# Performance work log

Hardware: AMD Instinct MI355X
Metric: run time of the kernel (lower is better)

The kernel has to match this reference:

```python
import jax, jax.numpy as jnp
import numpy as np

N = 100000
E = 1000000
F_NODE = 64
F_EDGE = 32
H = 128
C_NODE = 12
C_EDGE = 4


def _glorot(key, shape):
    fan_in, fan_out = shape[0], shape[1]
    s = (6.0 / (fan_in + fan_out)) ** 0.5
    return jax.random.uniform(key, shape, jnp.float32, -s, s)


def setup_inputs() -> dict:
    key = jax.random.key(0)
    ks = jax.random.split(key, 16)
    x = jax.random.normal(ks[0], (N, F_NODE), jnp.float32)
    edge_index = jax.random.randint(ks[1], (2, E), 0, N, jnp.int32)
    edge_attr = jax.random.normal(ks[2], (E, F_EDGE), jnp.float32)
    return {
        "x": x,
        "edge_index": edge_index,
        "edge_attr": edge_attr,
        "We": _glorot(ks[3], (F_NODE, H)), "be": jnp.zeros((H,), jnp.float32),
        "Wc1": _glorot(ks[4], (H, H)), "bc1": jnp.zeros((H,), jnp.float32),
        "Wc2": _glorot(ks[5], (H, H)), "bc2": jnp.zeros((H,), jnp.float32),
        "Wn1": _glorot(ks[6], (H, H // 2)), "bn1": jnp.zeros((H // 2,), jnp.float32),
        "Wn2": _glorot(ks[7], (H // 2, C_NODE)), "bn2": jnp.zeros((C_NODE,), jnp.float32),
        "Wedge1": _glorot(ks[8], (2 * H + F_EDGE, H)), "bedge1": jnp.zeros((H,), jnp.float32),
        "Wedge2": _glorot(ks[9], (H, C_EDGE)), "bedge2": jnp.zeros((C_EDGE,), jnp.float32),
    }


def _gcn_conv(x, W, b, src, tgt, n):
    # PyG GCNConv: add self-loops, symmetric deg normalization, scatter-add.
    xw = x @ W  # [N, H]
    loop = jnp.arange(n, dtype=src.dtype)
    s = jnp.concatenate([src, loop])
    t = jnp.concatenate([tgt, loop])
    deg = jax.ops.segment_sum(jnp.ones_like(t, jnp.float32), t, num_segments=n)
    dinv = jnp.where(deg > 0, jax.lax.rsqrt(jnp.maximum(deg, 1.0)), 0.0)
    norm = dinv[s] * dinv[t]  # [E+N]
    msg = xw[s] * norm[:, None]
    return jax.ops.segment_sum(msg, t, num_segments=n) + b


def reference(x, edge_index, edge_attr, We, be, Wc1, bc1, Wc2, bc2,
              Wn1, bn1, Wn2, bn2, Wedge1, bedge1, Wedge2, bedge2):
    n = x.shape[0]
    row, col = edge_index[0], edge_index[1]
    h = jax.nn.relu(x @ We + be)          # node_embed Linear+ReLU
    h = jax.nn.relu(h)                     # extra F.relu in forward
    h = jax.nn.relu(_gcn_conv(h, Wc1, bc1, row, col, n))
    h = jax.nn.relu(_gcn_conv(h, Wc2, bc2, row, col, n))
    node_logits = jax.nn.relu(h @ Wn1 + bn1) @ Wn2 + bn2
    e = jnp.concatenate([h[row], h[col], edge_attr], axis=-1)  # [E, 2H+Fe]
    edge_logits = jax.nn.relu(e @ Wedge1 + bedge1) @ Wedge2 + bedge2
    return (node_logits, edge_logits)
```

## Files before the change

kernel.cpp:

```cpp
#include <hip/hip_runtime.h>

#define N_NODES 100000
#define N_EDGES 1000000
#define NB_SCAN 391
#define EDGE_OUT_BASE 1200000

typedef __attribute__((ext_vector_type(8))) short short8;
typedef __attribute__((ext_vector_type(4))) unsigned short us4;
typedef __attribute__((ext_vector_type(4))) float f32x4;

__device__ __forceinline__ float bf2f(unsigned short u) {
    unsigned int x = ((unsigned int)u) << 16;
    return __builtin_bit_cast(float, x);
}
__device__ __forceinline__ float lo_bf(unsigned int u) {
    return __builtin_bit_cast(float, u << 16);
}
__device__ __forceinline__ float hi_bf(unsigned int u) {
    return __builtin_bit_cast(float, u & 0xffff0000u);
}
__device__ __forceinline__ unsigned short f2bf(float f) {
    unsigned int x = __builtin_bit_cast(unsigned int, f);
    return (unsigned short)((x + 0x7fffu + ((x >> 16) & 1u)) >> 16);
}

__global__ __launch_bounds__(256) void k_detect(const unsigned short* __restrict__ xr,
                                                int* __restrict__ flag) {
    __shared__ int s[256];
    int t = threadIdx.x;
    int cnt = 0;
    for (int i = t; i < 8192; i += 256) {
        int e = (xr[i] >> 7) & 0xFF;
        if (e >= 148) cnt++;
    }
    s[t] = cnt;
    __syncthreads();
    for (int off = 128; off > 0; off >>= 1) {
        if (t < off) s[t] += s[t + off];
        __syncthreads();
    }
    if (t == 0) *flag = (s[0] > 100) ? 1 : 0;
}

struct WPack { const void* p[14]; };
#define W_TOTAL 87888
__global__ __launch_bounds__(256) void k_convw(WPack wp, const int* __restrict__ flag,
                                               unsigned short* __restrict__ dst) {
    const int starts[15] = {0, 8192, 8320, 24704, 24832, 41216, 41344, 49536,
                            49600, 50368, 50380, 87244, 87372, 87884, 87888};
    bool f32 = (*flag != 0);
    int i = blockIdx.x * 256 + threadIdx.x;
    if (i >= W_TOTAL) return;
    int s = 0;
#pragma unroll
    for (int k = 1; k < 14; k++) s += (i >= starts[k]) ? 1 : 0;
    int j = i - starts[s];
    dst[i] = f32 ? f2bf(((const float*)wp.p[s])[j]) : ((const unsigned short*)wp.p[s])[j];
}
#define OW_We 0
#define OW_be 8192
#define OW_Wc1 8320
#define OW_bc1 24704
#define OW_Wc2 24832
#define OW_bc2 41216
#define OW_Wn1 41344
#define OW_bn1 49536
#define OW_Wn2 49600
#define OW_bn2 50368
#define OW_We1 50380
#define OW_be1 87244
#define OW_We2 87372
#define OW_be2 87884

__global__ __launch_bounds__(256) void k_hist(const int* __restrict__ ecol, int* __restrict__ deg) {
    int e = blockIdx.x * 256 + threadIdx.x;
    if (e < N_EDGES) atomicAdd(&deg[ecol[e]], 1);
}

__global__ __launch_bounds__(256) void k_scanA(const int* __restrict__ deg, int* __restrict__ bsum) {
    __shared__ int s[256];
    int i = blockIdx.x * 256 + threadIdx.x;
    s[threadIdx.x] = (i < N_NODES) ? deg[i] : 0;
    __syncthreads();
    for (int off = 128; off > 0; off >>= 1) {
        if (threadIdx.x < off) s[threadIdx.x] += s[threadIdx.x + off];
        __syncthreads();
    }
    if (threadIdx.x == 0) bsum[blockIdx.x] = s[0];
}

__global__ __launch_bounds__(512) void k_scanB(int* __restrict__ bsum) {
    __shared__ int s[512];
    int t = threadIdx.x;
    int v = (t < NB_SCAN) ? bsum[t] : 0;
    s[t] = v;
    __syncthreads();
    for (int off = 1; off < 512; off <<= 1) {
        int x = (t >= off) ? s[t - off] : 0;
        __syncthreads();
        s[t] += x;
        __syncthreads();
    }
    if (t < NB_SCAN) bsum[t] = s[t] - v;
}

__global__ __launch_bounds__(256) void k_scanC(const int* __restrict__ deg, const int* __restrict__ bsum,
                                               int* __restrict__ row_off, int* __restrict__ cursor,
                                               float* __restrict__ dinv) {
    __shared__ int s[256];
    int i = blockIdx.x * 256 + threadIdx.x;
    int t = threadIdx.x;
    int v = (i < N_NODES) ? deg[i] : 0;
    s[t] = v;
    __syncthreads();
    for (int off = 1; off < 256; off <<= 1) {
        int x = (t >= off) ? s[t - off] : 0;
        __syncthreads();
        s[t] += x;
        __syncthreads();
    }
    int excl = s[t] - v + bsum[blockIdx.x];
    if (i < N_NODES) {
        row_off[i] = excl;
        cursor[i] = excl;
        dinv[i] = rsqrtf((float)(v + 1));
    }
    if (i == N_NODES - 1) row_off[N_NODES] = excl + v;
}

__global__ __launch_bounds__(256) void k_fill(const int* __restrict__ erow, const int* __restrict__ ecol,
                                              int* __restrict__ cursor, int* __restrict__ csr,
                                              int2* __restrict__ aux) {
    int e = blockIdx.x * 256 + threadIdx.x;
    if (e < N_EDGES) {
        int c = ecol[e];
        int pos = atomicAdd(&cursor[c], 1);
        csr[pos] = erow[e];
        aux[pos] = make_int2(e, c);
    }
}

template <int K, int O, bool RELU, bool BIAS, bool SCALE>
__global__ __launch_bounds__(256) void gemm_rows(const void* __restrict__ A, int M,
                                                 const unsigned short* __restrict__ W, int o_real,
                                                 const unsigned short* __restrict__ bias,
                                                 void* __restrict__ Out, int out_pitch,
                                                 const float* __restrict__ rowscale,
                                                 const int* aflag, const int* oflag) {
    constexpr int KP = K + 8;
    constexpr int KS = K / 32;
    constexpr int OT = O / 16;
    __shared__ short wt[O * KP];
    __shared__ float bias_s[O];
    int tid = threadIdx.x;
    for (int idx = tid; idx < K * O; idx += 256) {
        int k = idx / O, o = idx % O;
        short w = 0;
        if (o < o_real) w = (short)W[(size_t)k * o_real + o];
        wt[o * KP + k] = w;
    }
    if (BIAS) {
        for (int o = tid; o < O; o += 256) bias_s[o] = (o < o_real) ? bf2f(bias[o]) : 0.f;
    }
    __syncthreads();

    bool af32 = aflag && (*aflag != 0);
    bool of32 = oflag && (*oflag != 0);

    int wid = tid >> 6, lane = tid & 63;
    int rbase = (blockIdx.x * 4 + wid) * 32;
    if (rbase >= M) return;
    int lq = lane >> 4, lr = lane & 15;

    short8 a[2][KS];
#pragma unroll
    for (int rg = 0; rg < 2; rg++) {
        int row = rbase + rg * 16 + lr;
        if (row >= M) row = M - 1;
        if (af32) {
            const float* ap = (const float*)A + (size_t)row * K + lq * 8;
#pragma unroll
            for (int ks = 0; ks < KS; ks++) {
                f32x4 u0 = *(const f32x4*)(ap + ks * 32);
                f32x4 u1 = *(const f32x4*)(ap + ks * 32 + 4);
                short8 v;
                v[0] = (short)f2bf(u0[0]); v[1] = (short)f2bf(u0[1]);
                v[2] = (short)f2bf(u0[2]); v[3] = (short)f2bf(u0[3]);
                v[4] = (short)f2bf(u1[0]); v[5] = (short)f2bf(u1[1]);
                v[6] = (short)f2bf(u1[2]); v[7] = (short)f2bf(u1[3]);
                a[rg][ks] = v;
            }
        } else {
            const unsigned short* ap = (const unsigned short*)A + (size_t)row * K + lq * 8;
#pragma unroll
            for (int ks = 0; ks < KS; ks++) a[rg][ks] = *(const short8*)(ap + ks * 32);
        }
    }

    f32x4 acc[2][OT];
#pragma unroll
    for (int rg = 0; rg < 2; rg++)
#pragma unroll
        for (int j = 0; j < OT; j++) {
            acc[rg][j][0] = 0.f; acc[rg][j][1] = 0.f; acc[rg][j][2] = 0.f; acc[rg][j][3] = 0.f;
        }

#pragma unroll
    for (int j = 0; j < OT; j++) {
        short8 b[KS];
#pragma unroll
        for (int ks = 0; ks < KS; ks++)
            b[ks] = *(const short8*)(&wt[(lr + 16 * j) * KP + ks * 32 + lq * 8]);
#pragma unroll
        for (int rg = 0; rg < 2; rg++)
#pragma unroll
            for (int ks = 0; ks < KS; ks++)
                acc[rg][j] = __builtin_amdgcn_mfma_f32_16x16x32_bf16(a[rg][ks], b[ks], acc[rg][j], 0, 0, 0);
    }

#pragma unroll
    for (int rg = 0; rg < 2; rg++)
#pragma unroll
        for (int j = 0; j < OT; j++)
#pragma unroll
            for (int r = 0; r < 4; r++) {
                int row = rbase + rg * 16 + lq * 4 + r;
                int col = lr + 16 * j;
                if (row < M && col < o_real) {
                    float v = acc[rg][j][r];
                    if (BIAS) v += bias_s[col];
                    if (RELU) v = fmaxf(v, 0.f);
                    if (SCALE) v *= rowscale[row];
                    size_t oi = (size_t)row * out_pitch + col;
                    if (of32) ((float*)Out)[oi] = v;
                    else ((unsigned short*)Out)[oi] = f2bf(v);
                }
            }
}

__global__ __launch_bounds__(256) void node_head(const unsigned short* __restrict__ A, int M,
                                                 const unsigned short* __restrict__ wbuf,
                                                 void* __restrict__ Out, const int* oflag) {
    __shared__ short wt1[64 * 136];
    __shared__ short zb[128 * 72];
    __shared__ short wt2[16 * 72];
    __shared__ float b1[64];
    __shared__ float b2[16];
    int tid = threadIdx.x;
    const unsigned short* Wn1 = wbuf + OW_Wn1;
    const unsigned short* Wn2 = wbuf + OW_Wn2;
    for (int idx = tid; idx < 64 * 128; idx += 256) {
        int k = idx >> 6, o = idx & 63;
        wt1[o * 136 + k] = (short)Wn1[idx];
    }
    for (int idx = tid; idx < 16 * 64; idx += 256) {
        int o = idx & 15, k = idx >> 4;
        wt2[o * 72 + k] = (o < 12) ? (short)Wn2[k * 12 + o] : 0;
    }
    if (tid < 64) b1[tid] = bf2f(wbuf[OW_bn1 + tid]);
    if (tid < 16) b2[tid] = (tid < 12) ? bf2f(wbuf[OW_bn2 + tid]) : 0.f;
    __syncthreads();

    bool of32 = oflag && (*oflag != 0);
    int wid = tid >> 6, lane = tid & 63;
    int lq = lane >> 4, lr = lane & 15;
    int rbase = blockIdx.x * 128 + wid * 32;

    short8 a[2][4];
#pragma unroll
    for (int rg = 0; rg < 2; rg++) {
        int row = rbase + rg * 16 + lr;
        if (row >= M) row = M - 1;
        const unsigned short* ap = A + (size_t)row * 128 + lq * 8;
#pragma unroll
        for (int ks = 0; ks < 4; ks++) a[rg][ks] = *(const short8*)(ap + ks * 32);
    }

    {
        f32x4 acc[2][4];
#pragma unroll
        for (int rg = 0; rg < 2; rg++)
#pragma unroll
            for (int j = 0; j < 4; j++) {
                acc[rg][j][0] = 0.f; acc[rg][j][1] = 0.f; acc[rg][j][2] = 0.f; acc[rg][j][3] = 0.f;
            }
#pragma unroll
        for (int j = 0; j < 4; j++) {
            short8 b[4];
#pragma unroll
            for (int ks = 0; ks < 4; ks++)
                b[ks] = *(const short8*)(&wt1[(lr + 16 * j) * 136 + ks * 32 + lq * 8]);
#pragma unroll
            for (int rg = 0; rg < 2; rg++)
#pragma unroll
                for (int ks = 0; ks < 4; ks++)
                    acc[rg][j] = __builtin_amdgcn_mfma_f32_16x16x32_bf16(a[rg][ks], b[ks], acc[rg][j], 0, 0, 0);
        }
#pragma unroll
        for (int rg = 0; rg < 2; rg++)
#pragma unroll
            for (int j = 0; j < 4; j++)
#pragma unroll
                for (int r = 0; r < 4; r++) {
                    int rl = wid * 32 + rg * 16 + lq * 4 + r;
                    int col = lr + 16 * j;
                    zb[rl * 72 + col] = (short)f2bf(fmaxf(acc[rg][j][r] + b1[col], 0.f));
                }
    }
    __syncthreads();

    {
        short8 a2[2][2];
#pragma unroll
        for (int rg = 0; rg < 2; rg++) {
            int rl = wid * 32 + rg * 16 + lr;
#pragma unroll
            for (int ks = 0; ks < 2; ks++)
                a2[rg][ks] = *(const short8*)(&zb[rl * 72 + ks * 32 + lq * 8]);
        }
        short8 b[2];
#pragma unroll
        for (int ks = 0; ks < 2; ks++)
            b[ks] = *(const short8*)(&wt2[lr * 72 + ks * 32 + lq * 8]);
        f32x4 acc[2];
#pragma unroll
        for (int rg = 0; rg < 2; rg++) {
            acc[rg][0] = 0.f; acc[rg][1] = 0.f; acc[rg][2] = 0.f; acc[rg][3] = 0.f;
#pragma unroll
            for (int ks = 0; ks < 2; ks++)
                acc[rg] = __builtin_amdgcn_mfma_f32_16x16x32_bf16(a2[rg][ks], b[ks], acc[rg], 0, 0, 0);
        }
#pragma unroll
        for (int rg = 0; rg < 2; rg++)
#pragma unroll
            for (int r = 0; r < 4; r++) {
                int row = rbase + rg * 16 + lq * 4 + r;
                int col = lr;
                if (row < M && col < 12) {
                    float v = acc[rg][r] + b2[col];
                    size_t oi = (size_t)row * 12 + col;
                    if (of32) ((float*)Out)[oi] = v;
                    else ((unsigned short*)Out)[oi] = f2bf(v);
                }
            }
    }
}

__global__ __launch_bounds__(256) void gemm_pq(const unsigned short* __restrict__ A, int M,
                                               const unsigned short* __restrict__ W1,
                                               const unsigned short* __restrict__ W2,
                                               unsigned short* __restrict__ Pout,
                                               unsigned short* __restrict__ Qout) {
    __shared__ short wt[128 * 136];
    int tid = threadIdx.x;
    int wid = tid >> 6, lane = tid & 63;
    int rbase = (blockIdx.x * 4 + wid) * 32;
    int lq = lane >> 4, lr = lane & 15;

    short8 a[2][4];
#pragma unroll
    for (int rg = 0; rg < 2; rg++) {
        int row = rbase + rg * 16 + lr;
        if (row >= M) row = M - 1;
        const unsigned short* ap = A + (size_t)row * 128 + lq * 8;
#pragma unroll
        for (int ks = 0; ks < 4; ks++) a[rg][ks] = *(const short8*)(ap + ks * 32);
    }

    int pc0 = (lr >> 2) * 32 + (lr & 3);

    for (int idx = tid; idx < 128 * 128; idx += 256) {
        int k = idx >> 7, o = idx & 127;
        wt[o * 136 + k] = (short)W1[idx];
    }
    __syncthreads();
    {
        f32x4 acc[2][8];
#pragma unroll
        for (int rg = 0; rg < 2; rg++)
#pragma unroll
            for (int j = 0; j < 8; j++) {
                acc[rg][j][0] = 0.f; acc[rg][j][1] = 0.f; acc[rg][j][2] = 0.f; acc[rg][j][3] = 0.f;
            }
#pragma unroll
        for (int j = 0; j < 8; j++) {
            short8 b[4];
#pragma unroll
            for (int ks = 0; ks < 4; ks++)
                b[ks] = *(const short8*)(&wt[(lr + 16 * j) * 136 + ks * 32 + lq * 8]);
#pragma unroll
            for (int rg = 0; rg < 2; rg++)
#pragma unroll
                for (int ks = 0; ks < 4; ks++)
                    acc[rg][j] = __builtin_amdgcn_mfma_f32_16x16x32_bf16(a[rg][ks], b[ks], acc[rg][j], 0, 0, 0);
        }
#pragma unroll
        for (int rg = 0; rg < 2; rg++)
#pragma unroll
            for (int j = 0; j < 8; j++)
#pragma unroll
                for (int r = 0; r < 4; r++) {
                    int row = rbase + rg * 16 + lq * 4 + r;
                    if (row < M) Pout[(size_t)row * 128 + pc0 + j * 4] = f2bf(acc[rg][j][r]);
                }
    }
    __syncthreads();

    for (int idx = tid; idx < 128 * 128; idx += 256) {
        int k = idx >> 7, o = idx & 127;
        wt[o * 136 + k] = (short)W2[idx];
    }
    __syncthreads();
    {
        f32x4 acc[2][8];
#pragma unroll
        for (int rg = 0; rg < 2; rg++)
#pragma unroll
            for (int j = 0; j < 8; j++) {
                acc[rg][j][0] = 0.f; acc[rg][j][1] = 0.f; acc[rg][j][2] = 0.f; acc[rg][j][3] = 0.f;
            }
#pragma unroll
        for (int j = 0; j < 8; j++) {
            short8 b[4];
#pragma unroll
            for (int ks = 0; ks < 4; ks++)
                b[ks] = *(const short8*)(&wt[(lr + 16 * j) * 136 + ks * 32 + lq * 8]);
#pragma unroll
            for (int rg = 0; rg < 2; rg++)
#pragma unroll
                for (int ks = 0; ks < 4; ks++)
                    acc[rg][j] = __builtin_amdgcn_mfma_f32_16x16x32_bf16(a[rg][ks], b[ks], acc[rg][j], 0, 0, 0);
        }
#pragma unroll
        for (int rg = 0; rg < 2; rg++)
#pragma unroll
            for (int j = 0; j < 8; j++)
#pragma unroll
                for (int r = 0; r < 4; r++) {
                    int row = rbase + rg * 16 + lq * 4 + r;
                    if (row < M) Qout[(size_t)row * 128 + pc0 + j * 4] = f2bf(acc[rg][j][r]);
                }
    }
}

__global__ __launch_bounds__(256) void conv_kernel(const unsigned short* __restrict__ xw_s,
                                                   const int* __restrict__ csr_src,
                                                   const int* __restrict__ row_off,
                                                   const float* __restrict__ dinv,
                                                   const unsigned short* __restrict__ bias,
                                                   unsigned short* __restrict__ out) {
    int wid = threadIdx.x >> 6, lane = threadIdx.x & 63;
    int base = (blockIdx.x * 4 + wid) * 2;
    int t0 = base, t1 = base + 1;
    int beg0 = row_off[t0], end0 = row_off[t0 + 1];
    int beg1 = row_off[t1], end1 = row_off[t1 + 1];
    float dt0 = dinv[t0], dt1 = dinv[t1];
    unsigned int v0 = *(const unsigned int*)(xw_s + (size_t)t0 * 128 + lane * 2);
    unsigned int v1 = *(const unsigned int*)(xw_s + (size_t)t1 * 128 + lane * 2);
    unsigned int bv = *(const unsigned int*)(bias + lane * 2);
    float a00 = lo_bf(v0), a01 = hi_bf(v0);
    float a10 = lo_bf(v1), a11 = hi_bf(v1);
    int i0 = beg0, i1 = beg1;
    while (i0 + 4 <= end0 && i1 + 4 <= end1) {
        int s00 = csr_src[i0], s01 = csr_src[i0 + 1], s02 = csr_src[i0 + 2], s03 = csr_src[i0 + 3];
        int s10 = csr_src[i1], s11 = csr_src[i1 + 1], s12 = csr_src[i1 + 2], s13 = csr_src[i1 + 3];
        unsigned int u00 = *(const unsigned int*)(xw_s + (size_t)s00 * 128 + lane * 2);
        unsigned int u01 = *(const unsigned int*)(xw_s + (size_t)s01 * 128 + lane * 2);
        unsigned int u02 = *(const unsigned int*)(xw_s + (size_t)s02 * 128 + lane * 2);
        unsigned int u03 = *(const unsigned int*)(xw_s + (size_t)s03 * 128 + lane * 2);
        unsigned int u10 = *(const unsigned int*)(xw_s + (size_t)s10 * 128 + lane * 2);
        unsigned int u11 = *(const unsigned int*)(xw_s + (size_t)s11 * 128 + lane * 2);
        unsigned int u12 = *(const unsigned int*)(xw_s + (size_t)s12 * 128 + lane * 2);
        unsigned int u13 = *(const unsigned int*)(xw_s + (size_t)s13 * 128 + lane * 2);
        a00 += lo_bf(u00) + lo_bf(u01) + lo_bf(u02) + lo_bf(u03);
        a01 += hi_bf(u00) + hi_bf(u01) + hi_bf(u02) + hi_bf(u03);
        a10 += lo_bf(u10) + lo_bf(u11) + lo_bf(u12) + lo_bf(u13);
        a11 += hi_bf(u10) + hi_bf(u11) + hi_bf(u12) + hi_bf(u13);
        i0 += 4; i1 += 4;
    }
    for (; i0 + 4 <= end0; i0 += 4) {
        int s0 = csr_src[i0], s1 = csr_src[i0 + 1], s2 = csr_src[i0 + 2], s3 = csr_src[i0 + 3];
        unsigned int u0 = *(const unsigned int*)(xw_s + (size_t)s0 * 128 + lane * 2);
        unsigned int u1 = *(const unsigned int*)(xw_s + (size_t)s1 * 128 + lane * 2);
        unsigned int u2 = *(const unsigned int*)(xw_s + (size_t)s2 * 128 + lane * 2);
        unsigned int u3 = *(const unsigned int*)(xw_s + (size_t)s3 * 128 + lane * 2);
        a00 += lo_bf(u0) + lo_bf(u1) + lo_bf(u2) + lo_bf(u3);
        a01 += hi_bf(u0) + hi_bf(u1) + hi_bf(u2) + hi_bf(u3);
    }
    for (; i1 + 4 <= end1; i1 += 4) {
        int s0 = csr_src[i1], s1 = csr_src[i1 + 1], s2 = csr_src[i1 + 2], s3 = csr_src[i1 + 3];
        unsigned int u0 = *(const unsigned int*)(xw_s + (size_t)s0 * 128 + lane * 2);
        unsigned int u1 = *(const unsigned int*)(xw_s + (size_t)s1 * 128 + lane * 2);
        unsigned int u2 = *(const unsigned int*)(xw_s + (size_t)s2 * 128 + lane * 2);
        unsigned int u3 = *(const unsigned int*)(xw_s + (size_t)s3 * 128 + lane * 2);
        a10 += lo_bf(u0) + lo_bf(u1) + lo_bf(u2) + lo_bf(u3);
        a11 += hi_bf(u0) + hi_bf(u1) + hi_bf(u2) + hi_bf(u3);
    }
    for (; i0 < end0; i0++) {
        int s = csr_src[i0];
        unsigned int u = *(const unsigned int*)(xw_s + (size_t)s * 128 + lane * 2);
        a00 += lo_bf(u); a01 += hi_bf(u);
    }
    for (; i1 < end1; i1++) {
        int s = csr_src[i1];
        unsigned int u = *(const unsigned int*)(xw_s + (size_t)s * 128 + lane * 2);
        a10 += lo_bf(u); a11 += hi_bf(u);
    }
    a00 = fmaxf(fmaf(a00, dt0, lo_bf(bv)), 0.f);
    a01 = fmaxf(fmaf(a01, dt0, hi_bf(bv)), 0.f);
    a10 = fmaxf(fmaf(a10, dt1, lo_bf(bv)), 0.f);
    a11 = fmaxf(fmaf(a11, dt1, hi_bf(bv)), 0.f);
    unsigned int o0 = (unsigned int)f2bf(a00) | ((unsigned int)f2bf(a01) << 16);
    unsigned int o1 = (unsigned int)f2bf(a10) | ((unsigned int)f2bf(a11) << 16);
    *(unsigned int*)(out + (size_t)t0 * 128 + lane * 2) = o0;
    *(unsigned int*)(out + (size_t)t1 * 128 + lane * 2) = o1;
}

__device__ __forceinline__ void epi_chunk(f32x4& ov, const f32x4& acc_lo, const f32x4& acc_hi,
                                          short8 pv, short8 qv,
                                          const float* __restrict__ b1s,
                                          const float* __restrict__ w2s, int pb) {
#pragma unroll
    for (int jj = 0; jj < 2; jj++) {
        const f32x4& ac = jj ? acc_hi : acc_lo;
#pragma unroll
        for (int r = 0; r < 4; r++) {
            int idx = jj * 4 + r;
            float t = ac[r] + bf2f((unsigned short)pv[idx]) + bf2f((unsigned short)qv[idx]) + b1s[pb + idx];
            t = fmaxf(t, 0.f);
            f32x4 w2v = *(const f32x4*)(&w2s[(pb + idx) * 4]);
            ov[0] = fmaf(t, w2v[0], ov[0]);
            ov[1] = fmaf(t, w2v[1], ov[1]);
            ov[2] = fmaf(t, w2v[2], ov[2]);
            ov[3] = fmaf(t, w2v[3], ov[3]);
        }
    }
}

__global__ __launch_bounds__(256) void edge_head(const void* __restrict__ ea,
                                                 const int* __restrict__ csr_src,
                                                 const int2* __restrict__ aux,
                                                 const unsigned short* __restrict__ P,
                                                 const unsigned short* __restrict__ Q,
                                                 const unsigned short* __restrict__ wbuf,
                                                 void* __restrict__ out, const int* dtflag) {
    __shared__ short wct[128 * 40];
    __shared__ float w2s[128 * 4];
    __shared__ float b1s[128];
    int tid = threadIdx.x;
    const unsigned short* Wc3 = wbuf + OW_We1 + 256 * 128;
    for (int idx = tid; idx < 32 * 128; idx += 256) {
        int k = idx >> 7, o = idx & 127;
        wct[o * 40 + k] = (short)Wc3[idx];
    }
    for (int idx = tid; idx < 512; idx += 256) {
        int p = idx >> 2, o = idx & 3;
        int ch = 16 * ((p & 31) >> 2) + 4 * (p >> 5) + (p & 3);
        w2s[idx] = bf2f(wbuf[OW_We2 + ch * 4 + o]);
    }
    if (tid < 128) {
        int p = tid;
        int ch = 16 * ((p & 31) >> 2) + 4 * (p >> 5) + (p & 3);
        b1s[p] = bf2f(wbuf[OW_be1 + ch]);
    }
    __syncthreads();

    bool f32io = (*dtflag != 0);
    int wid = tid >> 6, lane = tid & 63;
    int lq = lane >> 4, lr = lane & 15;
    int tbase = (blockIdx.x * 4 + wid) * 2;
    int p0a = tbase * 16, p0b = p0a + 16;

    int posa = p0a + lr, posb = p0b + lr;
    bool va = posa < N_EDGES, vb = posb < N_EDGES;
    int pca = va ? posa : (N_EDGES - 1);
    int pcb = vb ? posb : (N_EDGES - 1);

    int rna = csr_src[pca], rnb = csr_src[pcb];
    int2 axa = aux[pca], axb = aux[pcb];
    int gea = axa.x, cna = axa.y;
    int geb = axb.x, cnb = axb.y;

    auto load_efrag = [&](int ge) -> short8 {
        short8 v;
        if (f32io) {
            const float* eap = (const float*)ea + (size_t)ge * 32 + lq * 8;
            f32x4 u0 = __builtin_nontemporal_load((const f32x4*)eap);
            f32x4 u1 = __builtin_nontemporal_load((const f32x4*)(eap + 4));
            v[0] = (short)f2bf(u0[0]); v[1] = (short)f2bf(u0[1]);
            v[2] = (short)f2bf(u0[2]); v[3] = (short)f2bf(u0[3]);
            v[4] = (short)f2bf(u1[0]); v[5] = (short)f2bf(u1[1]);
            v[6] = (short)f2bf(u1[2]); v[7] = (short)f2bf(u1[3]);
        } else {
            v = __builtin_nontemporal_load((const short8*)((const unsigned short*)ea + (size_t)ge * 32 + lq * 8));
        }
        return v;
    };
    short8 efA = load_efrag(gea);
    short8 efB = load_efrag(geb);

    const unsigned short* PpA = P + (size_t)rna * 128 + lq * 32;
    const unsigned short* QpA = Q + (size_t)cna * 128 + lq * 32;
    const unsigned short* PpB = P + (size_t)rnb * 128 + lq * 32;
    const unsigned short* QpB = Q + (size_t)cnb * 128 + lq * 32;

    f32x4 zero; zero[0] = 0.f; zero[1] = 0.f; zero[2] = 0.f; zero[3] = 0.f;
    f32x4 ovA = zero, ovB = zero;

    {
        short8 pA0 = *(const short8*)(PpA + 0);
        short8 pA1 = *(const short8*)(PpA + 8);
        short8 qA0 = *(const short8*)(QpA + 0);
        short8 qA1 = *(const short8*)(QpA + 8);
        short8 pB0 = *(const short8*)(PpB + 0);
        short8 pB1 = *(const short8*)(PpB + 8);
        short8 qB0 = *(const short8*)(QpB + 0);
        short8 qB1 = *(const short8*)(QpB + 8);
        short8 wf0 = *(const short8*)(&wct[(0 * 16 + lr) * 40 + lq * 8]);
        short8 wf1 = *(const short8*)(&wct[(1 * 16 + lr) * 40 + lq * 8]);
        short8 wf2 = *(const short8*)(&wct[(2 * 16 + lr) * 40 + lq * 8]);
        short8 wf3 = *(const short8*)(&wct[(3 * 16 + lr) * 40 + lq * 8]);
        f32x4 aA0 = __builtin_amdgcn_mfma_f32_16x16x32_bf16(wf0, efA, zero, 0, 0, 0);
        f32x4 aA1 = __builtin_amdgcn_mfma_f32_16x16x32_bf16(wf1, efA, zero, 0, 0, 0);
        f32x4 aA2 = __builtin_amdgcn_mfma_f32_16x16x32_bf16(wf2, efA, zero, 0, 0, 0);
        f32x4 aA3 = __builtin_amdgcn_mfma_f32_16x16x32_bf16(wf3, efA, zero, 0, 0, 0);
        f32x4 aB0 = __builtin_amdgcn_mfma_f32_16x16x32_bf16(wf0, efB, zero, 0, 0, 0);
        f32x4 aB1 = __builtin_amdgcn_mfma_f32_16x16x32_bf16(wf1, efB, zero, 0, 0, 0);
        f32x4 aB2 = __builtin_amdgcn_mfma_f32_16x16x32_bf16(wf2, efB, zero, 0, 0, 0);
        f32x4 aB3 = __builtin_amdgcn_mfma_f32_16x16x32_bf16(wf3, efB, zero, 0, 0, 0);
        epi_chunk(ovA, aA0, aA1, pA0, qA0, b1s, w2s, lq * 32 + 0);
        epi_chunk(ovA, aA2, aA3, pA1, qA1, b1s, w2s, lq * 32 + 8);
        epi_chunk(ovB, aB0, aB1, pB0, qB0, b1s, w2s, lq * 32 + 0);
        epi_chunk(ovB, aB2, aB3, pB1, qB1, b1s, w2s, lq * 32 + 8);
    }
    {
        short8 pA0 = *(const short8*)(PpA + 16);
        short8 pA1 = *(const short8*)(PpA + 24);
        short8 qA0 = *(const short8*)(QpA + 16);
        short8 qA1 = *(const short8*)(QpA + 24);
        short8 pB0 = *(const short8*)(PpB + 16);
        short8 pB1 = *(const short8*)(PpB + 24);
        short8 qB0 = *(const short8*)(QpB + 16);
        short8 qB1 = *(const short8*)(QpB + 24);
        short8 wf0 = *(const short8*)(&wct[(4 * 16 + lr) * 40 + lq * 8]);
        short8 wf1 = *(const short8*)(&wct[(5 * 16 + lr) * 40 + lq * 8]);
        short8 wf2 = *(const short8*)(&wct[(6 * 16 + lr) * 40 + lq * 8]);
        short8 wf3 = *(const short8*)(&wct[(7 * 16 + lr) * 40 + lq * 8]);
        f32x4 aA0 = __builtin_amdgcn_mfma_f32_16x16x32_bf16(wf0, efA, zero, 0, 0, 0);
        f32x4 aA1 = __builtin_amdgcn_mfma_f32_16x16x32_bf16(wf1, efA, zero, 0, 0, 0);
        f32x4 aA2 = __builtin_amdgcn_mfma_f32_16x16x32_bf16(wf2, efA, zero, 0, 0, 0);
        f32x4 aA3 = __builtin_amdgcn_mfma_f32_16x16x32_bf16(wf3, efA, zero, 0, 0, 0);
        f32x4 aB0 = __builtin_amdgcn_mfma_f32_16x16x32_bf16(wf0, efB, zero, 0, 0, 0);
        f32x4 aB1 = __builtin_amdgcn_mfma_f32_16x16x32_bf16(wf1, efB, zero, 0, 0, 0);
        f32x4 aB2 = __builtin_amdgcn_mfma_f32_16x16x32_bf16(wf2, efB, zero, 0, 0, 0);
        f32x4 aB3 = __builtin_amdgcn_mfma_f32_16x16x32_bf16(wf3, efB, zero, 0, 0, 0);
        epi_chunk(ovA, aA0, aA1, pA0, qA0, b1s, w2s, lq * 32 + 16);
        epi_chunk(ovA, aA2, aA3, pA1, qA1, b1s, w2s, lq * 32 + 24);
        epi_chunk(ovB, aB0, aB1, pB0, qB0, b1s, w2s, lq * 32 + 16);
        epi_chunk(ovB, aB2, aB3, pB1, qB1, b1s, w2s, lq * 32 + 24);
    }

#pragma unroll
    for (int c = 0; c < 4; c++) {
        ovA[c] += __shfl_xor(ovA[c], 16);
        ovA[c] += __shfl_xor(ovA[c], 32);
        ovB[c] += __shfl_xor(ovB[c], 16);
        ovB[c] += __shfl_xor(ovB[c], 32);
    }
    if (lq == 0) {
        float be2_0 = bf2f(wbuf[OW_be2 + 0]), be2_1 = bf2f(wbuf[OW_be2 + 1]);
        float be2_2 = bf2f(wbuf[OW_be2 + 2]), be2_3 = bf2f(wbuf[OW_be2 + 3]);
        if (va) {
            size_t oi = (size_t)EDGE_OUT_BASE + (size_t)gea * 4;
            if (f32io) {
                f32x4 res; res[0] = ovA[0] + be2_0; res[1] = ovA[1] + be2_1;
                res[2] = ovA[2] + be2_2; res[3] = ovA[3] + be2_3;
                __builtin_nontemporal_store(res, (f32x4*)((float*)out + oi));
            } else {
                us4 res; res[0] = f2bf(ovA[0] + be2_0); res[1] = f2bf(ovA[1] + be2_1);
                res[2] = f2bf(ovA[2] + be2_2); res[3] = f2bf(ovA[3] + be2_3);
                __builtin_nontemporal_store(res, (us4*)((unsigned short*)out + oi));
            }
        }
        if (vb) {
            size_t oi = (size_t)EDGE_OUT_BASE + (size_t)geb * 4;
            if (f32io) {
                f32x4 res; res[0] = ovB[0] + be2_0; res[1] = ovB[1] + be2_1;
                res[2] = ovB[2] + be2_2; res[3] = ovB[3] + be2_3;
                __builtin_nontemporal_store(res, (f32x4*)((float*)out + oi));
            } else {
                us4 res; res[0] = f2bf(ovB[0] + be2_0); res[1] = f2bf(ovB[1] + be2_1);
                res[2] = f2bf(ovB[2] + be2_2); res[3] = f2bf(ovB[3] + be2_3);
                __builtin_nontemporal_store(res, (us4*)((unsigned short*)out + oi));
            }
        }
    }
}

extern "C" void kernel_launch(void* const* d_in, const int* in_sizes, int n_in,
                              void* d_out, int out_size, void* d_ws, size_t ws_size,
                              hipStream_t stream) {
    const void* x = d_in[0];
    const int* ei = (const int*)d_in[1];
    const void* ea = d_in[2];
    const int* erow = ei;
    const int* ecol = ei + N_EDGES;

    char* ws = (char*)d_ws;
    size_t off = 0;
    auto alloc = [&](size_t bytes) -> void* {
        void* p = ws + off;
        off += (bytes + 255) & ~(size_t)255;
        return p;
    };
    unsigned short* Abuf = (unsigned short*)alloc((size_t)N_NODES * 128 * 2);
    unsigned short* Bbuf = (unsigned short*)alloc((size_t)N_NODES * 128 * 2);
    int* deg = (int*)alloc((size_t)N_NODES * 4);
    int* row_off = (int*)alloc((size_t)(N_NODES + 1) * 4);
    int* cursor = (int*)alloc((size_t)N_NODES * 4);
    int* csr = (int*)alloc((size_t)N_EDGES * 4);
    int2* aux = (int2*)alloc((size_t)N_EDGES * 8);
    int* bsum = (int*)alloc(512 * 4);
    float* dinv = (float*)alloc((size_t)N_NODES * 4);
    unsigned short* wbuf = (unsigned short*)alloc((size_t)W_TOTAL * 2);
    int* dtflag = (int*)alloc(256);

    k_detect<<<1, 256, 0, stream>>>((const unsigned short*)x, dtflag);

    WPack wp;
    for (int i = 0; i < 14; i++) wp.p[i] = d_in[3 + i];
    k_convw<<<(W_TOTAL + 255) / 256, 256, 0, stream>>>(wp, dtflag, wbuf);

    (void)hipMemsetAsync(deg, 0, (size_t)N_NODES * 4, stream);
    k_hist<<<(N_EDGES + 255) / 256, 256, 0, stream>>>(ecol, deg);
    k_scanA<<<NB_SCAN, 256, 0, stream>>>(deg, bsum);
    k_scanB<<<1, 512, 0, stream>>>(bsum);
    k_scanC<<<NB_SCAN, 256, 0, stream>>>(deg, bsum, row_off, cursor, dinv);
    k_fill<<<(N_EDGES + 255) / 256, 256, 0, stream>>>(erow, ecol, cursor, csr, aux);

    int gB = (N_NODES + 127) / 128;
    gemm_rows<64, 128, true, true, false><<<gB, 256, 0, stream>>>(x, N_NODES, wbuf + OW_We, 128, wbuf + OW_be, Abuf, 128, nullptr, dtflag, nullptr);
    gemm_rows<128, 128, false, false, true><<<gB, 256, 0, stream>>>(Abuf, N_NODES, wbuf + OW_Wc1, 128, nullptr, Bbuf, 128, dinv, nullptr, nullptr);
    conv_kernel<<<N_NODES / 8, 256, 0, stream>>>(Bbuf, csr, row_off, dinv, wbuf + OW_bc1, Abuf);
    gemm_rows<128, 128, false, false, true><<<gB, 256, 0, stream>>>(Abuf, N_NODES, wbuf + OW_Wc2, 128, nullptr, Bbuf, 128, dinv, nullptr, nullptr);
    conv_kernel<<<N_NODES / 8, 256, 0, stream>>>(Bbuf, csr, row_off, dinv, wbuf + OW_bc2, Abuf);
    node_head<<<gB, 256, 0, stream>>>(Abuf, N_NODES, wbuf, d_out, dtflag);
    gemm_pq<<<gB, 256, 0, stream>>>(Abuf, N_NODES, wbuf + OW_We1, wbuf + OW_We1 + 128 * 128, Bbuf, Abuf);
    edge_head<<<(N_EDGES + 127) / 128, 256, 0, stream>>>(ea, csr, aux, Bbuf, Abuf, wbuf, d_out, dtflag);
}
```

Measured before the change: 530.9 us.

## Process four contiguous CSR rows per wave with double-buffered gather loads

The GCN aggregation kernel now assigns four consecutive target nodes to each wavefront. It walks their combined contiguous CSR edge range in chunks of eight, loading the next chunk into a second register buffer while the current one is accumulated. Each edge is routed to the right node's accumulator by comparing its position against the row boundaries. This is meant to remove imbalanced per-row tail loops and keep more independent gathers in flight, at the cost of more registers, per-edge branching, and clamped redundant loads at the range end.

```diff
diff --git a/kernel.cpp b/kernel.cpp
--- a/kernel.cpp
+++ b/kernel.cpp
@@ -443,6 +443,24 @@
     }
 }
 
+#define CONV_LOADC(U, base)                                                             \
+    _Pragma("unroll") for (int k = 0; k < 8; k++) {                                     \
+        int p = (base) + k;                                                             \
+        int pc = (p < cend) ? p : (cend - 1);                                           \
+        int s = csr_src[pc];                                                            \
+        U[k] = *(const unsigned int*)(xw_s + (size_t)s * 128 + lane * 2);               \
+    }
+#define CONV_CONSUME(U, base)                                                           \
+    _Pragma("unroll") for (int k = 0; k < 8; k++) {                                     \
+        int p = (base) + k;                                                             \
+        if (p < cend) {                                                                 \
+            float lo = lo_bf(U[k]), hi = hi_bf(U[k]);                                   \
+            if (p >= b3)      { A3l += lo; A3h += hi; }                                 \
+            else if (p >= b2) { A2l += lo; A2h += hi; }                                 \
+            else if (p >= b1) { A1l += lo; A1h += hi; }                                 \
+            else              { A0l += lo; A0h += hi; }                                 \
+        }                                                                               \
+    }
 __global__ __launch_bounds__(256) void conv_kernel(const unsigned short* __restrict__ xw_s,
                                                    const int* __restrict__ csr_src,
                                                    const int* __restrict__ row_off,
@@ -450,70 +468,52 @@
                                                    const unsigned short* __restrict__ bias,
                                                    unsigned short* __restrict__ out) {
     int wid = threadIdx.x >> 6, lane = threadIdx.x & 63;
-    int base = (blockIdx.x * 4 + wid) * 2;
-    int t0 = base, t1 = base + 1;
-    int beg0 = row_off[t0], end0 = row_off[t0 + 1];
-    int beg1 = row_off[t1], end1 = row_off[t1 + 1];
-    float dt0 = dinv[t0], dt1 = dinv[t1];
-    unsigned int v0 = *(const unsigned int*)(xw_s + (size_t)t0 * 128 + lane * 2);
-    unsigned int v1 = *(const unsigned int*)(xw_s + (size_t)t1 * 128 + lane * 2);
+    int t0 = (blockIdx.x * 4 + wid) * 4;
+    int b0 = row_off[t0], b1 = row_off[t0 + 1], b2 = row_off[t0 + 2];
+    int b3 = row_off[t0 + 3], cend = row_off[t0 + 4];
+
+    unsigned int v0 = *(const unsigned int*)(xw_s + (size_t)(t0 + 0) * 128 + lane * 2);
+    unsigned int v1 = *(const unsigned int*)(xw_s + (size_t)(t0 + 1) * 128 + lane * 2);
+    unsigned int v2 = *(const unsigned int*)(xw_s + (size_t)(t0 + 2) * 128 + lane * 2);
+    unsigned int v3 = *(const unsigned int*)(xw_s + (size_t)(t0 + 3) * 128 + lane * 2);
+    float A0l = lo_bf(v0), A0h = hi_bf(v0);
+    float A1l = lo_bf(v1), A1h = hi_bf(v1);
+    float A2l = lo_bf(v2), A2h = hi_bf(v2);
+    float A3l = lo_bf(v3), A3h = hi_bf(v3);
+
+    if (b0 < cend) {
+        unsigned int UA[8], UB[8];
+        int i = b0;
+        CONV_LOADC(UA, i);
+        while (true) {
+            bool hasB = (i + 8) < cend;
+            if (hasB) { CONV_LOADC(UB, i + 8); }
+            CONV_CONSUME(UA, i);
+            i += 8;
+            if (!hasB) break;
+            bool hasA = (i + 8) < cend;
+            if (hasA) { CONV_LOADC(UA, i + 8); }
+            CONV_CONSUME(UB, i);
+            i += 8;
+            if (!hasA) break;
+        }
+    }
+
     unsigned int bv = *(const unsigned int*)(bias + lane * 2);
-    float a00 = lo_bf(v0), a01 = hi_bf(v0);
-    float a10 = lo_bf(v1), a11 = hi_bf(v1);
-    int i0 = beg0, i1 = beg1;
-    while (i0 + 4 <= end0 && i1 + 4 <= end1) {
-        int s00 = csr_src[i0], s01 = csr_src[i0 + 1], s02 = csr_src[i0 + 2], s03 = csr_src[i0 + 3];
-        int s10 = csr_src[i1], s11 = csr_src[i1 + 1], s12 = csr_src[i1 + 2], s13 = csr_src[i1 + 3];
-        unsigned int u00 = *(const unsigned int*)(xw_s + (size_t)s00 * 128 + lane * 2);
-        unsigned int u01 = *(const unsigned int*)(xw_s + (size_t)s01 * 128 + lane * 2);
-        unsigned int u02 = *(const unsigned int*)(xw_s + (size_t)s02 * 128 + lane * 2);
-        unsigned int u03 = *(const unsigned int*)(xw_s + (size_t)s03 * 128 + lane * 2);
-        unsigned int u10 = *(const unsigned int*)(xw_s + (size_t)s10 * 128 + lane * 2);
-        unsigned int u11 = *(const unsigned int*)(xw_s + (size_t)s11 * 128 + lane * 2);
-        unsigned int u12 = *(const unsigned int*)(xw_s + (size_t)s12 * 128 + lane * 2);
-        unsigned int u13 = *(const unsigned int*)(xw_s + (size_t)s13 * 128 + lane * 2);
-        a00 += lo_bf(u00) + lo_bf(u01) + lo_bf(u02) + lo_bf(u03);
-        a01 += hi_bf(u00) + hi_bf(u01) + hi_bf(u02) + hi_bf(u03);
-        a10 += lo_bf(u10) + lo_bf(u11) + lo_bf(u12) + lo_bf(u13);
-        a11 += hi_bf(u10) + hi_bf(u11) + hi_bf(u12) + hi_bf(u13);
-        i0 += 4; i1 += 4;
-    }
-    for (; i0 + 4 <= end0; i0 += 4) {
-        int s0 = csr_src[i0], s1 = csr_src[i0 + 1], s2 = csr_src[i0 + 2], s3 = csr_src[i0 + 3];
-        unsigned int u0 = *(const unsigned int*)(xw_s + (size_t)s0 * 128 + lane * 2);
-        unsigned int u1 = *(const unsigned int*)(xw_s + (size_t)s1 * 128 + lane * 2);
-        unsigned int u2 = *(const unsigned int*)(xw_s + (size_t)s2 * 128 + lane * 2);
-        unsigned int u3 = *(const unsigned int*)(xw_s + (size_t)s3 * 128 + lane * 2);
-        a00 += lo_bf(u0) + lo_bf(u1) + lo_bf(u2) + lo_bf(u3);
-        a01 += hi_bf(u0) + hi_bf(u1) + hi_bf(u2) + hi_bf(u3);
-    }
-    for (; i1 + 4 <= end1; i1 += 4) {
-        int s0 = csr_src[i1], s1 = csr_src[i1 + 1], s2 = csr_src[i1 + 2], s3 = csr_src[i1 + 3];
-        unsigned int u0 = *(const unsigned int*)(xw_s + (size_t)s0 * 128 + lane * 2);
-        unsigned int u1 = *(const unsigned int*)(xw_s + (size_t)s1 * 128 + lane * 2);
-        unsigned int u2 = *(const unsigned int*)(xw_s + (size_t)s2 * 128 + lane * 2);
-        unsigned int u3 = *(const unsigned int*)(xw_s + (size_t)s3 * 128 + lane * 2);
-        a10 += lo_bf(u0) + lo_bf(u1) + lo_bf(u2) + lo_bf(u3);
-        a11 += hi_bf(u0) + hi_bf(u1) + hi_bf(u2) + hi_bf(u3);
-    }
-    for (; i0 < end0; i0++) {
-        int s = csr_src[i0];
-        unsigned int u = *(const unsigned int*)(xw_s + (size_t)s * 128 + lane * 2);
-        a00 += lo_bf(u); a01 += hi_bf(u);
-    }
-    for (; i1 < end1; i1++) {
-        int s = csr_src[i1];
-        unsigned int u = *(const unsigned int*)(xw_s + (size_t)s * 128 + lane * 2);
-        a10 += lo_bf(u); a11 += hi_bf(u);
-    }
-    a00 = fmaxf(fmaf(a00, dt0, lo_bf(bv)), 0.f);
-    a01 = fmaxf(fmaf(a01, dt0, hi_bf(bv)), 0.f);
-    a10 = fmaxf(fmaf(a10, dt1, lo_bf(bv)), 0.f);
-    a11 = fmaxf(fmaf(a11, dt1, hi_bf(bv)), 0.f);
-    unsigned int o0 = (unsigned int)f2bf(a00) | ((unsigned int)f2bf(a01) << 16);
-    unsigned int o1 = (unsigned int)f2bf(a10) | ((unsigned int)f2bf(a11) << 16);
-    *(unsigned int*)(out + (size_t)t0 * 128 + lane * 2) = o0;
-    *(unsigned int*)(out + (size_t)t1 * 128 + lane * 2) = o1;
+    float bl = lo_bf(bv), bh = hi_bf(bv);
+    float d0 = dinv[t0], d1 = dinv[t0 + 1], d2 = dinv[t0 + 2], d3 = dinv[t0 + 3];
+    A0l = fmaxf(fmaf(A0l, d0, bl), 0.f); A0h = fmaxf(fmaf(A0h, d0, bh), 0.f);
+    A1l = fmaxf(fmaf(A1l, d1, bl), 0.f); A1h = fmaxf(fmaf(A1h, d1, bh), 0.f);
+    A2l = fmaxf(fmaf(A2l, d2, bl), 0.f); A2h = fmaxf(fmaf(A2h, d2, bh), 0.f);
+    A3l = fmaxf(fmaf(A3l, d3, bl), 0.f); A3h = fmaxf(fmaf(A3h, d3, bh), 0.f);
+    *(unsigned int*)(out + (size_t)(t0 + 0) * 128 + lane * 2) =
+        (unsigned int)f2bf(A0l) | ((unsigned int)f2bf(A0h) << 16);
+    *(unsigned int*)(out + (size_t)(t0 + 1) * 128 + lane * 2) =
+        (unsigned int)f2bf(A1l) | ((unsigned int)f2bf(A1h) << 16);
+    *(unsigned int*)(out + (size_t)(t0 + 2) * 128 + lane * 2) =
+        (unsigned int)f2bf(A2l) | ((unsigned int)f2bf(A2h) << 16);
+    *(unsigned int*)(out + (size_t)(t0 + 3) * 128 + lane * 2) =
+        (unsigned int)f2bf(A3l) | ((unsigned int)f2bf(A3h) << 16);
 }
 
 __device__ __forceinline__ void epi_chunk(f32x4& ov, const f32x4& acc_lo, const f32x4& acc_hi,
@@ -741,9 +741,9 @@
     int gB = (N_NODES + 127) / 128;
     gemm_rows<64, 128, true, true, false><<<gB, 256, 0, stream>>>(x, N_NODES, wbuf + OW_We, 128, wbuf + OW_be, Abuf, 128, nullptr, dtflag, nullptr);
     gemm_rows<128, 128, false, false, true><<<gB, 256, 0, stream>>>(Abuf, N_NODES, wbuf + OW_Wc1, 128, nullptr, Bbuf, 128, dinv, nullptr, nullptr);
-    conv_kernel<<<N_NODES / 8, 256, 0, stream>>>(Bbuf, csr, row_off, dinv, wbuf + OW_bc1, Abuf);
+    conv_kernel<<<N_NODES / 16, 256, 0, stream>>>(Bbuf, csr, row_off, dinv, wbuf + OW_bc1, Abuf);
     gemm_rows<128, 128, false, false, true><<<gB, 256, 0, stream>>>(Abuf, N_NODES, wbuf + OW_Wc2, 128, nullptr, Bbuf, 128, dinv, nullptr, nullptr);
-    conv_kernel<<<N_NODES / 8, 256, 0, stream>>>(Bbuf, csr, row_off, dinv, wbuf + OW_bc2, Abuf);
+    conv_kernel<<<N_NODES / 16, 256, 0, stream>>>(Bbuf, csr, row_off, dinv, wbuf + OW_bc2, Abuf);
     node_head<<<gB, 256, 0, stream>>>(Abuf, N_NODES, wbuf, d_out, dtflag);
     gemm_pq<<<gB, 256, 0, stream>>>(Abuf, N_NODES, wbuf + OW_We1, wbuf + OW_We1 + 128 * 128, Bbuf, Abuf);
     edge_head<<<(N_EDGES + 127) / 128, 256, 0, stream>>>(ea, csr, aux, Bbuf, Abuf, wbuf, d_out, dtflag);
```

After: 547.8 us. +3.2%, slower.
